# Performance work log

Measured on AMD Instinct MI355X. Metric: run time of the kernel, lower is better.

## Reference

```python
import math
import jax, jax.numpy as jnp
import numpy as np

N, T, D, H = 256, 128, 1024, 1024


def setup_inputs() -> dict:
    key = jax.random.key(0)
    k1, k2, k3, k4, k5 = jax.random.split(key, 5)
    x = jax.random.normal(k1, (N, T, D), dtype=jnp.float32)
    A = jax.random.normal(k2, (N, H, 4, 4), dtype=jnp.float32)
    Wx = jax.random.normal(k3, (D, 4 * H), dtype=jnp.float32) / math.sqrt(D)
    Wh = jax.random.normal(k4, (H, 4 * H), dtype=jnp.float32) / math.sqrt(H)
    Wattn = jax.random.normal(k5, (H, 4 * H), dtype=jnp.float32) / math.sqrt(H)
    b = jnp.zeros((4 * H,), dtype=jnp.float32)
    return {"x": x, "A": A, "Wx": Wx, "Wh": Wh, "Wattn": Wattn, "b": b}


def reference(x, A, Wx, Wh, Wattn, b):
    n, t, d = x.shape
    h = A.shape[1]
    A_flat = A.reshape(n, h, -1)            # (N, H, 16)
    h0 = A_flat.mean(axis=-1)               # mean over 4x4 grid
    c0 = h0
    scale = 1.0 / math.sqrt(h)

    def step(carry, xt):
        prev_h, prev_c = carry
        # scaled dot-product attention over the 16 spatial locations
        scores = jnp.einsum('nh,nhl->nl', prev_h, A_flat) * scale  # (N, 16)
        w = jax.nn.softmax(scores, axis=1)
        attn = jnp.einsum('nhl,nl->nh', A_flat, w)                 # (N, H)
        pre = xt @ Wx + prev_h @ Wh + attn @ Wattn + b             # (N, 4H)
        ai, af, ao, ag = jnp.split(pre, 4, axis=1)
        i = jax.nn.sigmoid(ai)
        f = jax.nn.sigmoid(af)
        o = jax.nn.sigmoid(ao)
        g = jnp.tanh(ag)
        next_c = f * prev_c + i * g
        next_h = o * jnp.tanh(next_c)
        return (next_h, next_c), next_h

    xs = jnp.swapaxes(x, 0, 1)               # (T, N, D)
    _, hs = jax.lax.scan(step, (h0, c0), xs)  # hs: (T, N, H)
    return jnp.swapaxes(hs, 0, 1)             # (N, T, H)
```

## Files before the change

### kernel.cpp

```cpp
#include <hip/hip_runtime.h>
#include <hip/hip_bf16.h>
#include <stdint.h>

#define N_ 256
#define T_ 128
#define D_ 1024
#define H_ 1024
#define FH_ 4096
#define K2_ 2048

typedef __bf16 bf16x8 __attribute__((ext_vector_type(8)));
typedef float f32x4 __attribute__((ext_vector_type(4)));

__global__ __launch_bounds__(256) void transpose_cast(
    const float* __restrict__ src, int cols,
    __hip_bfloat16* __restrict__ dst, int dst_stride, int dst_coloff)
{
    __shared__ float tile[32][33];
    int cb = blockIdx.x * 32, rb = blockIdx.y * 32;
    int tx = threadIdx.x, ty = threadIdx.y;
#pragma unroll
    for (int i = 0; i < 4; i++)
        tile[ty + i * 8][tx] = src[(size_t)(rb + ty + i * 8) * cols + cb + tx];
    __syncthreads();
#pragma unroll
    for (int i = 0; i < 4; i++)
        dst[(size_t)(cb + ty + i * 8) * dst_stride + dst_coloff + rb + tx] =
            __float2bfloat16(tile[tx][ty + i * 8]);
}

#define BM 64
#define BN 128
#define BK 64
#define BKP 72

__global__ __launch_bounds__(256) void gemm_x(
    const float* __restrict__ Xf,
    const __hip_bfloat16* __restrict__ BT,
    __hip_bfloat16* __restrict__ Cp, int t0)
{
    __shared__ __hip_bfloat16 Al[BM][BKP];
    __shared__ __hip_bfloat16 Bl[BN][BKP];
    const int tid = threadIdx.x;
    const int lane = tid & 63, wid = tid >> 6;
    const int m0 = blockIdx.y * BM, n0 = blockIdx.x * BN;
    const int wm = (wid >> 1) * 32, wn = (wid & 1) * 64;
    const int rs = tid >> 3, kc = (tid & 7) * 8;
    f32x4 acc[2][4] = {};

    for (int k0 = 0; k0 < D_; k0 += BK) {
#pragma unroll
        for (int p = 0; p < BM; p += 32) {
            int r = rs + p;
            int g = m0 + r;
            int nn = g & 255, tl = g >> 8;
            const float* s = Xf + ((size_t)nn * T_ + (t0 + tl)) * D_ + k0 + kc;
            float4 v0 = *reinterpret_cast<const float4*>(s);
            float4 v1 = *reinterpret_cast<const float4*>(s + 4);
            __hip_bfloat16 h8[8];
            h8[0] = __float2bfloat16(v0.x); h8[1] = __float2bfloat16(v0.y);
            h8[2] = __float2bfloat16(v0.z); h8[3] = __float2bfloat16(v0.w);
            h8[4] = __float2bfloat16(v1.x); h8[5] = __float2bfloat16(v1.y);
            h8[6] = __float2bfloat16(v1.z); h8[7] = __float2bfloat16(v1.w);
            *reinterpret_cast<int4*>(&Al[r][kc]) = *reinterpret_cast<const int4*>(h8);
        }
#pragma unroll
        for (int p = 0; p < BN; p += 32) {
            int r = rs + p;
            const __hip_bfloat16* s = BT + (size_t)(n0 + r) * D_ + k0 + kc;
            *reinterpret_cast<int4*>(&Bl[r][kc]) = *reinterpret_cast<const int4*>(s);
        }
        __syncthreads();
        const int ko = (lane >> 4) * 8;
#pragma unroll
        for (int kk = 0; kk < BK; kk += 32) {
            bf16x8 a0 = *reinterpret_cast<const bf16x8*>(&Al[wm + (lane & 15)][kk + ko]);
            bf16x8 a1 = *reinterpret_cast<const bf16x8*>(&Al[wm + 16 + (lane & 15)][kk + ko]);
#pragma unroll
            for (int ni = 0; ni < 4; ni++) {
                bf16x8 bq = *reinterpret_cast<const bf16x8*>(&Bl[wn + ni * 16 + (lane & 15)][kk + ko]);
                acc[0][ni] = __builtin_amdgcn_mfma_f32_16x16x32_bf16(a0, bq, acc[0][ni], 0, 0, 0);
                acc[1][ni] = __builtin_amdgcn_mfma_f32_16x16x32_bf16(a1, bq, acc[1][ni], 0, 0, 0);
            }
        }
        __syncthreads();
    }
    const int cr = (lane >> 4) * 4, ccol = lane & 15;
#pragma unroll
    for (int mi = 0; mi < 2; mi++)
#pragma unroll
        for (int ni = 0; ni < 4; ni++)
#pragma unroll
            for (int r = 0; r < 4; r++) {
                size_t idx = (size_t)(m0 + wm + mi * 16 + cr + r) * FH_ + (n0 + wn + ni * 16 + ccol);
                Cp[idx] = __float2bfloat16(acc[mi][ni][r]);
            }
}

__global__ __launch_bounds__(256) void abf_cast(
    const float* __restrict__ A, __hip_bfloat16* __restrict__ Abf)
{
    size_t i = ((size_t)blockIdx.x * 256 + threadIdx.x) * 4;
    float4 v = *reinterpret_cast<const float4*>(A + i);
    __hip_bfloat16 o[4];
    o[0] = __float2bfloat16(v.x); o[1] = __float2bfloat16(v.y);
    o[2] = __float2bfloat16(v.z); o[3] = __float2bfloat16(v.w);
    *reinterpret_cast<uint2*>(Abf + i) = *reinterpret_cast<uint2*>(o);
}

__global__ __launch_bounds__(256) void init_p(
    const float* __restrict__ A, float* __restrict__ cbuf,
    __hip_bfloat16* __restrict__ hb0)
{
    const int n = blockIdx.x, tid = threadIdx.x;
    float hv[4];
#pragma unroll
    for (int q = 0; q < 4; q++) {
        const float4* Ap = reinterpret_cast<const float4*>(A + ((size_t)n * H_ + tid * 4 + q) * 16);
        float4 q0 = Ap[0], q1 = Ap[1], q2 = Ap[2], q3 = Ap[3];
        float s = q0.x + q0.y + q0.z + q0.w + q1.x + q1.y + q1.z + q1.w
                + q2.x + q2.y + q2.z + q2.w + q3.x + q3.y + q3.z + q3.w;
        hv[q] = s * 0.0625f;
    }
    *reinterpret_cast<float4*>(cbuf + (size_t)n * H_ + tid * 4) = *reinterpret_cast<float4*>(hv);
    __hip_bfloat16 h4[4];
#pragma unroll
    for (int q = 0; q < 4; q++) h4[q] = __float2bfloat16(hv[q]);
    *reinterpret_cast<uint2*>(hb0 + (size_t)n * K2_ + tid * 4) = *reinterpret_cast<uint2*>(h4);
}

__global__ __launch_bounds__(256) void wattn2(
    __hip_bfloat16* __restrict__ hbt,
    const __hip_bfloat16* __restrict__ Abf)
{
    __shared__ float red[4][16];
    const int n = blockIdx.x, tid = threadIdx.x;
    const int lane = tid & 63, wv4 = tid >> 6;

    float h4[4];
    {
        uint2 hraw = *reinterpret_cast<const uint2*>(hbt + (size_t)n * K2_ + tid * 4);
        __hip_bfloat16 hb4[4];
        *reinterpret_cast<uint2*>(hb4) = hraw;
#pragma unroll
        for (int q = 0; q < 4; q++) h4[q] = __bfloat162float(hb4[q]);
    }
    bf16x8 a[4][2];
    const __hip_bfloat16* ap = Abf + ((size_t)n * H_ + tid * 4) * 16;
#pragma unroll
    for (int q = 0; q < 4; q++) {
        a[q][0] = *reinterpret_cast<const bf16x8*>(ap + q * 16);
        a[q][1] = *reinterpret_cast<const bf16x8*>(ap + q * 16 + 8);
    }
    float spv[16];
#pragma unroll
    for (int l = 0; l < 8; l++) {
        spv[l]     = h4[0] * (float)a[0][0][l] + h4[1] * (float)a[1][0][l]
                   + h4[2] * (float)a[2][0][l] + h4[3] * (float)a[3][0][l];
        spv[l + 8] = h4[0] * (float)a[0][1][l] + h4[1] * (float)a[1][1][l]
                   + h4[2] * (float)a[2][1][l] + h4[3] * (float)a[3][1][l];
    }
#pragma unroll
    for (int l = 0; l < 16; l++) {
        spv[l] += __shfl_xor(spv[l], 1);  spv[l] += __shfl_xor(spv[l], 2);
        spv[l] += __shfl_xor(spv[l], 4);  spv[l] += __shfl_xor(spv[l], 8);
        spv[l] += __shfl_xor(spv[l], 16); spv[l] += __shfl_xor(spv[l], 32);
    }
    if (lane == 0) {
#pragma unroll
        for (int l = 0; l < 16; l++) red[wv4][l] = spv[l];
    }
    __syncthreads();
    float w[16], se = 0.f;
    {
        float sc[16], m;
#pragma unroll
        for (int l = 0; l < 16; l++)
            sc[l] = (red[0][l] + red[1][l] + red[2][l] + red[3][l]) * 0.03125f;
        m = sc[0];
#pragma unroll
        for (int l = 1; l < 16; l++) m = fmaxf(m, sc[l]);
#pragma unroll
        for (int l = 0; l < 16; l++) { w[l] = __expf(sc[l] - m); se += w[l]; }
        float inv = 1.f / se;
#pragma unroll
        for (int l = 0; l < 16; l++) w[l] *= inv;
    }
    __hip_bfloat16 o4[4];
#pragma unroll
    for (int q = 0; q < 4; q++) {
        float s = 0.f;
#pragma unroll
        for (int l = 0; l < 8; l++) s += w[l] * (float)a[q][0][l];
#pragma unroll
        for (int l = 0; l < 8; l++) s += w[l + 8] * (float)a[q][1][l];
        o4[q] = __float2bfloat16(s);
    }
    *reinterpret_cast<uint2*>(hbt + (size_t)n * K2_ + H_ + tid * 4) =
        *reinterpret_cast<uint2*>(o4);
}

#define LDAp 136

__global__ __launch_bounds__(512) void step_gemm(
    const __hip_bfloat16* __restrict__ hb_in,
    __hip_bfloat16* __restrict__ hb_out,
    const __hip_bfloat16* __restrict__ W2T,
    const __hip_bfloat16* __restrict__ xp,
    const float* __restrict__ bias,
    float* __restrict__ cbuf,
    float* __restrict__ out, int t)
{
    __shared__ __align__(16) char smem[69632];
    float* pls = (float*)smem;

    const int tid = threadIdx.x;
    const int lane = tid & 63, wv = tid >> 6;
    const int bid = blockIdx.x;
    const int q = bid >> 3;
    const int ct = (bid & 7) + 8 * (q >> 2);
    const int r  = q & 3;
    const int hc0 = ct * 16, n0 = r * 64;
    const int rs = tid >> 4;
    const int kc = (tid & 15) * 8;
    const int l15 = lane & 15, ko8 = (lane >> 4) * 8;
    const int wm = (wv >> 1) * 16, wn = (wv & 1) * 32;

    const int gB0 = ((rs) >> 4) * 1024 + hc0 + (rs & 15);
    const int gB1 = ((rs + 32) >> 4) * 1024 + hc0 + ((rs + 32) & 15);
    const __hip_bfloat16* aS0 = hb_in + (size_t)(n0 + rs) * K2_ + kc;
    const __hip_bfloat16* aS1 = hb_in + (size_t)(n0 + rs + 32) * K2_ + kc;
    const __hip_bfloat16* bS0 = W2T + (size_t)gB0 * K2_ + kc;
    const __hip_bfloat16* bS1 = W2T + (size_t)gB1 * K2_ + kc;

    int4 ra0, ra1, rb0, rb1;
    auto LOAD = [&](int k0) {
        ra0 = *reinterpret_cast<const int4*>(aS0 + k0);
        ra1 = *reinterpret_cast<const int4*>(aS1 + k0);
        rb0 = *reinterpret_cast<const int4*>(bS0 + k0);
        rb1 = *reinterpret_cast<const int4*>(bS1 + k0);
    };
    auto WRITE = [&](int b) {
        __hip_bfloat16* Al = (__hip_bfloat16*)(smem + b * 17408);
        __hip_bfloat16* Bl = (__hip_bfloat16*)(smem + 34816 + b * 17408);
        *reinterpret_cast<int4*>(Al + rs * LDAp + kc) = ra0;
        *reinterpret_cast<int4*>(Al + (rs + 32) * LDAp + kc) = ra1;
        *reinterpret_cast<int4*>(Bl + rs * LDAp + kc) = rb0;
        *reinterpret_cast<int4*>(Bl + (rs + 32) * LDAp + kc) = rb1;
    };

    LOAD(0);
    WRITE(0);
    __syncthreads();

    f32x4 acc0{}, acc1{};
#pragma unroll 1
    for (int it = 0; it < 16; ++it) {
        if (it < 15) LOAD((it + 1) * 128);
        const int cur = it & 1;
        const __hip_bfloat16* pA  = (const __hip_bfloat16*)(smem + cur * 17408) + (wm + l15) * LDAp + ko8;
        const __hip_bfloat16* pB0 = (const __hip_bfloat16*)(smem + 34816 + cur * 17408) + (wn + l15) * LDAp + ko8;
        const __hip_bfloat16* pB1 = pB0 + 16 * LDAp;
#pragma unroll
        for (int kf = 0; kf < 4; kf++) {
            bf16x8 af = *reinterpret_cast<const bf16x8*>(pA + kf * 32);
            bf16x8 b0 = *reinterpret_cast<const bf16x8*>(pB0 + kf * 32);
            bf16x8 b1 = *reinterpret_cast<const bf16x8*>(pB1 + kf * 32);
            acc0 = __builtin_amdgcn_mfma_f32_16x16x32_bf16(af, b0, acc0, 0, 0, 0);
            acc1 = __builtin_amdgcn_mfma_f32_16x16x32_bf16(af, b1, acc1, 0, 0, 0);
        }
        __syncthreads();
        if (it < 15) {
            WRITE(cur ^ 1);
            __syncthreads();
        }
    }

    {
        const int cr = (lane >> 4) * 4;
#pragma unroll
        for (int r4 = 0; r4 < 4; r4++) {
            pls[(wm + cr + r4) * 68 + wn + l15]      = acc0[r4];
            pls[(wm + cr + r4) * 68 + wn + 16 + l15] = acc1[r4];
        }
    }
    __syncthreads();

    {
        const int n_l = tid >> 3, c2 = (tid & 7) * 2;
        const int nn = n0 + n_l;
        float hv2[2], cv2[2];
        const size_t cbase = (size_t)nn * H_ + hc0 + c2;
        float2 cold = *reinterpret_cast<const float2*>(cbuf + cbase);
        cv2[0] = cold.x; cv2[1] = cold.y;
#pragma unroll
        for (int cc = 0; cc < 2; cc++) {
            const int c = c2 + cc;
            float pre[4];
#pragma unroll
            for (int s = 0; s < 4; s++) {
                const int gj = s * 1024 + hc0 + c;
                pre[s] = pls[n_l * 68 + s * 16 + c]
                       + __bfloat162float(xp[(size_t)nn * FH_ + gj]) + bias[gj];
            }
            float iv = 1.f / (1.f + __expf(-pre[0]));
            float fv = 1.f / (1.f + __expf(-pre[1]));
            float ov = 1.f / (1.f + __expf(-pre[2]));
            float gx = fminf(fmaxf(pre[3], -20.f), 20.f);
            float eg = __expf(2.f * gx);
            float gv = (eg - 1.f) / (eg + 1.f);
            float c2v = fv * cv2[cc] + iv * gv;
            cv2[cc] = c2v;
            float cx = fminf(fmaxf(c2v, -20.f), 20.f);
            float ec = __expf(2.f * cx);
            hv2[cc] = ov * (ec - 1.f) / (ec + 1.f);
        }
        *reinterpret_cast<float2*>(cbuf + cbase) = make_float2(cv2[0], cv2[1]);
        *reinterpret_cast<float2*>(out + ((size_t)nn * T_ + t) * H_ + hc0 + c2) =
            make_float2(hv2[0], hv2[1]);
        __hip_bfloat16 h2[2];
        h2[0] = __float2bfloat16(hv2[0]);
        h2[1] = __float2bfloat16(hv2[1]);
        *reinterpret_cast<uint32_t*>(hb_out + (size_t)nn * K2_ + hc0 + c2) =
            *reinterpret_cast<uint32_t*>(h2);
    }
}

extern "C" void kernel_launch(void* const* d_in, const int* in_sizes, int n_in,
                              void* d_out, int out_size, void* d_ws, size_t ws_size,
                              hipStream_t stream)
{
    const float* x     = (const float*)d_in[0];
    const float* A     = (const float*)d_in[1];
    const float* Wx    = (const float*)d_in[2];
    const float* Wh    = (const float*)d_in[3];
    const float* Wattn = (const float*)d_in[4];
    const float* b     = (const float*)d_in[5];
    float* out = (float*)d_out;
    char* ws = (char*)d_ws;
    dim3 tb(32, 8);

    const size_t SZ_W2T = (size_t)FH_ * K2_ * 2;
    const size_t SZ_WxT = (size_t)FH_ * D_ * 2;
    const size_t SZ_Abf = (size_t)N_ * H_ * 16 * 2;
    const size_t SZ_HB  = (size_t)N_ * K2_ * 2;
    const size_t SZ_C   = (size_t)N_ * H_ * 4;
    const size_t SZ_XPT = (size_t)N_ * FH_ * 2;

    size_t off = 0;
    __hip_bfloat16* W2T = (__hip_bfloat16*)(ws + off); off += SZ_W2T;
    __hip_bfloat16* WxT = (__hip_bfloat16*)(ws + off); off += SZ_WxT;
    __hip_bfloat16* Abf = (__hip_bfloat16*)(ws + off); off += SZ_Abf;
    __hip_bfloat16* hbA = (__hip_bfloat16*)(ws + off); off += SZ_HB;
    __hip_bfloat16* hbB = (__hip_bfloat16*)(ws + off); off += SZ_HB;
    float* cbuf = (float*)(ws + off); off += SZ_C;
    __hip_bfloat16* xpb = (__hip_bfloat16*)(ws + off);

    size_t rem = (ws_size > off) ? (ws_size - off) : 0;
    int TC = 64;
    while (TC > 1 && (size_t)TC * SZ_XPT > rem) TC >>= 1;

    transpose_cast<<<dim3(FH_ / 32, H_ / 32), tb, 0, stream>>>(Wh, FH_, W2T, K2_, 0);
    transpose_cast<<<dim3(FH_ / 32, H_ / 32), tb, 0, stream>>>(Wattn, FH_, W2T, K2_, H_);
    transpose_cast<<<dim3(FH_ / 32, D_ / 32), tb, 0, stream>>>(Wx, FH_, WxT, D_, 0);
    abf_cast<<<dim3((N_ * H_ * 16) / 1024), 256, 0, stream>>>(A, Abf);
    init_p<<<N_, 256, 0, stream>>>(A, cbuf, hbA);

    __hip_bfloat16* hbp[2] = {hbA, hbB};
    for (int t0 = 0; t0 < T_; t0 += TC) {
        int tc = (T_ - t0 < TC) ? (T_ - t0) : TC;
        gemm_x<<<dim3(FH_ / BN, tc * N_ / BM), 256, 0, stream>>>(x, WxT, xpb, t0);
        for (int tl = 0; tl < tc; tl++) {
            int t = t0 + tl;
            wattn2<<<N_, 256, 0, stream>>>(hbp[t & 1], Abf);
            step_gemm<<<dim3(256), 512, 0, stream>>>(
                hbp[t & 1], hbp[(t + 1) & 1], W2T,
                xpb + (size_t)tl * N_ * FH_, b, cbuf, out, t);
        }
    }
}
```

Baseline: 3.113 ms.

## Precompute A·Wattn per batch and fuse attention into step kernel

Uses linearity to precompute AW = A_flat^T·Wattn per batch (N×4H×16) once, so each step's attention contribution becomes a 16-term weighted sum of AW with the softmax weights. This halves the recurrent GEMM K dimension from 2048 to 1024. It also removes the separate per-step wattn kernel: the step kernel emits partial attention scores for the next step, and the next step reduces them. The trade-off is a large extra per-step read of AW (256×4096×16 bf16) in the epilogue. The WaT scratch also aliases the xp buffer, which is safe only because aw_gemm runs before gemm_x.

```diff
diff --git a/kernel.cpp b/kernel.cpp
--- a/kernel.cpp
+++ b/kernel.cpp
@@ -7,7 +7,6 @@
 #define D_ 1024
 #define H_ 1024
 #define FH_ 4096
-#define K2_ 2048
 
 typedef __bf16 bf16x8 __attribute__((ext_vector_type(8)));
 typedef float f32x4 __attribute__((ext_vector_type(4)));
@@ -97,6 +96,55 @@
             }
 }
 
+__global__ __launch_bounds__(256) void aw_gemm(
+    const float* __restrict__ A, const __hip_bfloat16* __restrict__ WaT,
+    __hip_bfloat16* __restrict__ AW)
+{
+    __shared__ __hip_bfloat16 Al[16][72];
+    __shared__ __hip_bfloat16 Bl[128][72];
+    const int tid = threadIdx.x, lane = tid & 63, wv = tid >> 6;
+    const int n = blockIdx.y, j0 = blockIdx.x * 128;
+    const int rs = tid >> 3, kc = (tid & 7) * 8;
+    f32x4 acc[2] = {};
+    for (int k0 = 0; k0 < 1024; k0 += 64) {
+        {
+            int h = tid >> 2, lq = (tid & 3) * 4;
+            float4 v = *reinterpret_cast<const float4*>(A + ((size_t)n * 1024 + k0 + h) * 16 + lq);
+            Al[lq + 0][h] = __float2bfloat16(v.x);
+            Al[lq + 1][h] = __float2bfloat16(v.y);
+            Al[lq + 2][h] = __float2bfloat16(v.z);
+            Al[lq + 3][h] = __float2bfloat16(v.w);
+        }
+#pragma unroll
+        for (int p = 0; p < 128; p += 32) {
+            int r = rs + p;
+            *reinterpret_cast<int4*>(&Bl[r][kc]) =
+                *reinterpret_cast<const int4*>(WaT + (size_t)(j0 + r) * 1024 + k0 + kc);
+        }
+        __syncthreads();
+        const int ko = (lane >> 4) * 8;
+#pragma unroll
+        for (int kk = 0; kk < 64; kk += 32) {
+            bf16x8 a0 = *reinterpret_cast<const bf16x8*>(&Al[lane & 15][kk + ko]);
+#pragma unroll
+            for (int nf = 0; nf < 2; nf++) {
+                bf16x8 bq = *reinterpret_cast<const bf16x8*>(&Bl[wv * 32 + nf * 16 + (lane & 15)][kk + ko]);
+                acc[nf] = __builtin_amdgcn_mfma_f32_16x16x32_bf16(a0, bq, acc[nf], 0, 0, 0);
+            }
+        }
+        __syncthreads();
+    }
+    const int cr = (lane >> 4) * 4, cc = lane & 15;
+#pragma unroll
+    for (int nf = 0; nf < 2; nf++) {
+        __hip_bfloat16 t4[4];
+#pragma unroll
+        for (int r = 0; r < 4; r++) t4[r] = __float2bfloat16(acc[nf][r]);
+        *reinterpret_cast<uint2*>(AW + ((size_t)n * 4096 + j0 + wv * 32 + nf * 16 + cc) * 16 + cr) =
+            *reinterpret_cast<uint2*>(t4);
+    }
+}
+
 __global__ __launch_bounds__(256) void abf_cast(
     const float* __restrict__ A, __hip_bfloat16* __restrict__ Abf)
 {
@@ -108,58 +156,37 @@
     *reinterpret_cast<uint2*>(Abf + i) = *reinterpret_cast<uint2*>(o);
 }
 
-__global__ __launch_bounds__(256) void init_p(
+__global__ __launch_bounds__(256) void init_s(
     const float* __restrict__ A, float* __restrict__ cbuf,
-    __hip_bfloat16* __restrict__ hb0)
-{
+    __hip_bfloat16* __restrict__ hb0, float* __restrict__ sp0)
+{
+    __shared__ float red[4][16];
     const int n = blockIdx.x, tid = threadIdx.x;
+    const int lane = tid & 63, wvv = tid >> 6;
+    float a[4][16];
     float hv[4];
 #pragma unroll
     for (int q = 0; q < 4; q++) {
         const float4* Ap = reinterpret_cast<const float4*>(A + ((size_t)n * H_ + tid * 4 + q) * 16);
         float4 q0 = Ap[0], q1 = Ap[1], q2 = Ap[2], q3 = Ap[3];
-        float s = q0.x + q0.y + q0.z + q0.w + q1.x + q1.y + q1.z + q1.w
-                + q2.x + q2.y + q2.z + q2.w + q3.x + q3.y + q3.z + q3.w;
+        a[q][0] = q0.x; a[q][1] = q0.y; a[q][2] = q0.z; a[q][3] = q0.w;
+        a[q][4] = q1.x; a[q][5] = q1.y; a[q][6] = q1.z; a[q][7] = q1.w;
+        a[q][8] = q2.x; a[q][9] = q2.y; a[q][10] = q2.z; a[q][11] = q2.w;
+        a[q][12] = q3.x; a[q][13] = q3.y; a[q][14] = q3.z; a[q][15] = q3.w;
+        float s = 0.f;
+#pragma unroll
+        for (int l = 0; l < 16; l++) s += a[q][l];
         hv[q] = s * 0.0625f;
     }
     *reinterpret_cast<float4*>(cbuf + (size_t)n * H_ + tid * 4) = *reinterpret_cast<float4*>(hv);
     __hip_bfloat16 h4[4];
 #pragma unroll
     for (int q = 0; q < 4; q++) h4[q] = __float2bfloat16(hv[q]);
-    *reinterpret_cast<uint2*>(hb0 + (size_t)n * K2_ + tid * 4) = *reinterpret_cast<uint2*>(h4);
-}
-
-__global__ __launch_bounds__(256) void wattn2(
-    __hip_bfloat16* __restrict__ hbt,
-    const __hip_bfloat16* __restrict__ Abf)
-{
-    __shared__ float red[4][16];
-    const int n = blockIdx.x, tid = threadIdx.x;
-    const int lane = tid & 63, wv4 = tid >> 6;
-
-    float h4[4];
-    {
-        uint2 hraw = *reinterpret_cast<const uint2*>(hbt + (size_t)n * K2_ + tid * 4);
-        __hip_bfloat16 hb4[4];
-        *reinterpret_cast<uint2*>(hb4) = hraw;
-#pragma unroll
-        for (int q = 0; q < 4; q++) h4[q] = __bfloat162float(hb4[q]);
-    }
-    bf16x8 a[4][2];
-    const __hip_bfloat16* ap = Abf + ((size_t)n * H_ + tid * 4) * 16;
-#pragma unroll
-    for (int q = 0; q < 4; q++) {
-        a[q][0] = *reinterpret_cast<const bf16x8*>(ap + q * 16);
-        a[q][1] = *reinterpret_cast<const bf16x8*>(ap + q * 16 + 8);
-    }
+    *reinterpret_cast<uint2*>(hb0 + (size_t)n * H_ + tid * 4) = *reinterpret_cast<uint2*>(h4);
     float spv[16];
 #pragma unroll
-    for (int l = 0; l < 8; l++) {
-        spv[l]     = h4[0] * (float)a[0][0][l] + h4[1] * (float)a[1][0][l]
-                   + h4[2] * (float)a[2][0][l] + h4[3] * (float)a[3][0][l];
-        spv[l + 8] = h4[0] * (float)a[0][1][l] + h4[1] * (float)a[1][1][l]
-                   + h4[2] * (float)a[2][1][l] + h4[3] * (float)a[3][1][l];
-    }
+    for (int l = 0; l < 16; l++)
+        spv[l] = hv[0] * a[0][l] + hv[1] * a[1][l] + hv[2] * a[2][l] + hv[3] * a[3][l];
 #pragma unroll
     for (int l = 0; l < 16; l++) {
         spv[l] += __shfl_xor(spv[l], 1);  spv[l] += __shfl_xor(spv[l], 2);
@@ -168,50 +195,36 @@
     }
     if (lane == 0) {
 #pragma unroll
-        for (int l = 0; l < 16; l++) red[wv4][l] = spv[l];
+        for (int l = 0; l < 16; l++) red[wvv][l] = spv[l];
     }
     __syncthreads();
-    float w[16], se = 0.f;
-    {
-        float sc[16], m;
-#pragma unroll
-        for (int l = 0; l < 16; l++)
-            sc[l] = (red[0][l] + red[1][l] + red[2][l] + red[3][l]) * 0.03125f;
-        m = sc[0];
-#pragma unroll
-        for (int l = 1; l < 16; l++) m = fmaxf(m, sc[l]);
-#pragma unroll
-        for (int l = 0; l < 16; l++) { w[l] = __expf(sc[l] - m); se += w[l]; }
-        float inv = 1.f / se;
-#pragma unroll
-        for (int l = 0; l < 16; l++) w[l] *= inv;
-    }
-    __hip_bfloat16 o4[4];
-#pragma unroll
-    for (int q = 0; q < 4; q++) {
-        float s = 0.f;
-#pragma unroll
-        for (int l = 0; l < 8; l++) s += w[l] * (float)a[q][0][l];
-#pragma unroll
-        for (int l = 0; l < 8; l++) s += w[l + 8] * (float)a[q][1][l];
-        o4[q] = __float2bfloat16(s);
-    }
-    *reinterpret_cast<uint2*>(hbt + (size_t)n * K2_ + H_ + tid * 4) =
-        *reinterpret_cast<uint2*>(o4);
+    float* spn = sp0 + (size_t)n * 1024;
+    if (tid < 16)
+        spn[tid] = red[0][tid] + red[1][tid] + red[2][tid] + red[3][tid];
+#pragma unroll
+    for (int j = 0; j < 4; j++) {
+        int idx = 16 + tid * 4 + j;
+        if (idx < 1024) spn[idx] = 0.f;
+    }
 }
 
 #define LDAp 136
 
-__global__ __launch_bounds__(512) void step_gemm(
+__global__ __launch_bounds__(512) void step_fused(
     const __hip_bfloat16* __restrict__ hb_in,
     __hip_bfloat16* __restrict__ hb_out,
-    const __hip_bfloat16* __restrict__ W2T,
+    const __hip_bfloat16* __restrict__ WhT,
+    const __hip_bfloat16* __restrict__ AW,
+    const __hip_bfloat16* __restrict__ Abf,
     const __hip_bfloat16* __restrict__ xp,
     const float* __restrict__ bias,
     float* __restrict__ cbuf,
+    const float* __restrict__ sp_in,
+    float* __restrict__ sp_out,
     float* __restrict__ out, int t)
 {
     __shared__ __align__(16) char smem[69632];
+    __shared__ float wl[64][16];
     float* pls = (float*)smem;
 
     const int tid = threadIdx.x;
@@ -226,12 +239,12 @@
     const int l15 = lane & 15, ko8 = (lane >> 4) * 8;
     const int wm = (wv >> 1) * 16, wn = (wv & 1) * 32;
 
-    const int gB0 = ((rs) >> 4) * 1024 + hc0 + (rs & 15);
-    const int gB1 = ((rs + 32) >> 4) * 1024 + hc0 + ((rs + 32) & 15);
-    const __hip_bfloat16* aS0 = hb_in + (size_t)(n0 + rs) * K2_ + kc;
-    const __hip_bfloat16* aS1 = hb_in + (size_t)(n0 + rs + 32) * K2_ + kc;
-    const __hip_bfloat16* bS0 = W2T + (size_t)gB0 * K2_ + kc;
-    const __hip_bfloat16* bS1 = W2T + (size_t)gB1 * K2_ + kc;
+    const int j0 = (rs >> 4) * 1024 + hc0 + (rs & 15);
+    const int j1 = ((rs + 32) >> 4) * 1024 + hc0 + ((rs + 32) & 15);
+    const __hip_bfloat16* aS0 = hb_in + (size_t)(n0 + rs) * H_ + kc;
+    const __hip_bfloat16* aS1 = hb_in + (size_t)(n0 + rs + 32) * H_ + kc;
+    const __hip_bfloat16* bS0 = WhT + (size_t)j0 * H_ + kc;
+    const __hip_bfloat16* bS1 = WhT + (size_t)j1 * H_ + kc;
 
     int4 ra0, ra1, rb0, rb1;
     auto LOAD = [&](int k0) {
@@ -249,14 +262,36 @@
         *reinterpret_cast<int4*>(Bl + (rs + 32) * LDAp + kc) = rb1;
     };
 
+    {
+        const int row8 = tid >> 3, l2 = (tid & 7) * 2;
+        const float* spn = sp_in + (size_t)(n0 + row8) * 1024 + l2;
+        float s0 = 0.f, s1 = 0.f;
+#pragma unroll 8
+        for (int cj = 0; cj < 64; cj++) {
+            float2 v = *reinterpret_cast<const float2*>(spn + cj * 16);
+            s0 += v.x; s1 += v.y;
+        }
+        s0 *= 0.03125f; s1 *= 0.03125f;
+        float m = fmaxf(s0, s1);
+        m = fmaxf(m, __shfl_xor(m, 1));
+        m = fmaxf(m, __shfl_xor(m, 2));
+        m = fmaxf(m, __shfl_xor(m, 4));
+        float e0 = __expf(s0 - m), e1 = __expf(s1 - m);
+        float se = e0 + e1;
+        se += __shfl_xor(se, 1); se += __shfl_xor(se, 2); se += __shfl_xor(se, 4);
+        float inv = 1.f / se;
+        wl[row8][l2] = e0 * inv;
+        wl[row8][l2 + 1] = e1 * inv;
+    }
+
     LOAD(0);
     WRITE(0);
     __syncthreads();
 
     f32x4 acc0{}, acc1{};
 #pragma unroll 1
-    for (int it = 0; it < 16; ++it) {
-        if (it < 15) LOAD((it + 1) * 128);
+    for (int it = 0; it < 8; ++it) {
+        if (it < 7) LOAD((it + 1) * 128);
         const int cur = it & 1;
         const __hip_bfloat16* pA  = (const __hip_bfloat16*)(smem + cur * 17408) + (wm + l15) * LDAp + ko8;
         const __hip_bfloat16* pB0 = (const __hip_bfloat16*)(smem + 34816 + cur * 17408) + (wn + l15) * LDAp + ko8;
@@ -270,7 +305,7 @@
             acc1 = __builtin_amdgcn_mfma_f32_16x16x32_bf16(af, b1, acc1, 0, 0, 0);
         }
         __syncthreads();
-        if (it < 15) {
+        if (it < 7) {
             WRITE(cur ^ 1);
             __syncthreads();
         }
@@ -289,24 +324,41 @@
     {
         const int n_l = tid >> 3, c2 = (tid & 7) * 2;
         const int nn = n0 + n_l;
+        float w[16];
+#pragma unroll
+        for (int l = 0; l < 16; l++) w[l] = wl[n_l][l];
+
+        float pre[4][2];
+#pragma unroll
+        for (int s = 0; s < 4; s++) {
+            const int gj = s * 1024 + hc0 + c2;
+            __hip_bfloat16 xb[2];
+            *reinterpret_cast<uint32_t*>(xb) =
+                *reinterpret_cast<const uint32_t*>(xp + (size_t)nn * FH_ + gj);
+            const __hip_bfloat16* awp = AW + ((size_t)nn * FH_ + gj) * 16;
+#pragma unroll
+            for (int cc = 0; cc < 2; cc++) {
+                bf16x8 w0 = *reinterpret_cast<const bf16x8*>(awp + cc * 16);
+                bf16x8 w1 = *reinterpret_cast<const bf16x8*>(awp + cc * 16 + 8);
+                float aw = 0.f;
+#pragma unroll
+                for (int l = 0; l < 8; l++) aw += w[l] * (float)w0[l];
+#pragma unroll
+                for (int l = 0; l < 8; l++) aw += w[l + 8] * (float)w1[l];
+                pre[s][cc] = pls[n_l * 68 + s * 16 + c2 + cc]
+                           + __bfloat162float(xb[cc]) + bias[gj + cc] + aw;
+            }
+        }
         float hv2[2], cv2[2];
         const size_t cbase = (size_t)nn * H_ + hc0 + c2;
         float2 cold = *reinterpret_cast<const float2*>(cbuf + cbase);
         cv2[0] = cold.x; cv2[1] = cold.y;
 #pragma unroll
         for (int cc = 0; cc < 2; cc++) {
-            const int c = c2 + cc;
-            float pre[4];
-#pragma unroll
-            for (int s = 0; s < 4; s++) {
-                const int gj = s * 1024 + hc0 + c;
-                pre[s] = pls[n_l * 68 + s * 16 + c]
-                       + __bfloat162float(xp[(size_t)nn * FH_ + gj]) + bias[gj];
-            }
-            float iv = 1.f / (1.f + __expf(-pre[0]));
-            float fv = 1.f / (1.f + __expf(-pre[1]));
-            float ov = 1.f / (1.f + __expf(-pre[2]));
-            float gx = fminf(fmaxf(pre[3], -20.f), 20.f);
+            float iv = 1.f / (1.f + __expf(-pre[0][cc]));
+            float fv = 1.f / (1.f + __expf(-pre[1][cc]));
+            float ov = 1.f / (1.f + __expf(-pre[2][cc]));
+            float gx = fminf(fmaxf(pre[3][cc], -20.f), 20.f);
             float eg = __expf(2.f * gx);
             float gv = (eg - 1.f) / (eg + 1.f);
             float c2v = fv * cv2[cc] + iv * gv;
@@ -321,8 +373,33 @@
         __hip_bfloat16 h2[2];
         h2[0] = __float2bfloat16(hv2[0]);
         h2[1] = __float2bfloat16(hv2[1]);
-        *reinterpret_cast<uint32_t*>(hb_out + (size_t)nn * K2_ + hc0 + c2) =
+        *reinterpret_cast<uint32_t*>(hb_out + (size_t)nn * H_ + hc0 + c2) =
             *reinterpret_cast<uint32_t*>(h2);
+
+        const __hip_bfloat16* ap = Abf + ((size_t)nn * H_ + hc0 + c2) * 16;
+        bf16x8 a00 = *reinterpret_cast<const bf16x8*>(ap);
+        bf16x8 a01 = *reinterpret_cast<const bf16x8*>(ap + 8);
+        bf16x8 a10 = *reinterpret_cast<const bf16x8*>(ap + 16);
+        bf16x8 a11 = *reinterpret_cast<const bf16x8*>(ap + 24);
+        float spv[16];
+#pragma unroll
+        for (int l = 0; l < 8; l++) {
+            spv[l]     = hv2[0] * (float)a00[l] + hv2[1] * (float)a10[l];
+            spv[l + 8] = hv2[0] * (float)a01[l] + hv2[1] * (float)a11[l];
+        }
+#pragma unroll
+        for (int l = 0; l < 16; l++) {
+            spv[l] += __shfl_xor(spv[l], 1);
+            spv[l] += __shfl_xor(spv[l], 2);
+            spv[l] += __shfl_xor(spv[l], 4);
+        }
+        if ((tid & 7) == 0) {
+            float* d = sp_out + ((size_t)nn * 64 + ct) * 16;
+            *reinterpret_cast<float4*>(d)      = *reinterpret_cast<float4*>(&spv[0]);
+            *reinterpret_cast<float4*>(d + 4)  = *reinterpret_cast<float4*>(&spv[4]);
+            *reinterpret_cast<float4*>(d + 8)  = *reinterpret_cast<float4*>(&spv[8]);
+            *reinterpret_cast<float4*>(d + 12) = *reinterpret_cast<float4*>(&spv[12]);
+        }
     }
 }
 
@@ -340,42 +417,50 @@
     char* ws = (char*)d_ws;
     dim3 tb(32, 8);
 
-    const size_t SZ_W2T = (size_t)FH_ * K2_ * 2;
+    const size_t SZ_WhT = (size_t)FH_ * H_ * 2;
     const size_t SZ_WxT = (size_t)FH_ * D_ * 2;
+    const size_t SZ_AW  = (size_t)N_ * FH_ * 16 * 2;
     const size_t SZ_Abf = (size_t)N_ * H_ * 16 * 2;
-    const size_t SZ_HB  = (size_t)N_ * K2_ * 2;
+    const size_t SZ_HB  = (size_t)N_ * H_ * 2;
     const size_t SZ_C   = (size_t)N_ * H_ * 4;
+    const size_t SZ_SP  = (size_t)N_ * 64 * 16 * 4;
     const size_t SZ_XPT = (size_t)N_ * FH_ * 2;
 
     size_t off = 0;
-    __hip_bfloat16* W2T = (__hip_bfloat16*)(ws + off); off += SZ_W2T;
+    __hip_bfloat16* WhT = (__hip_bfloat16*)(ws + off); off += SZ_WhT;
     __hip_bfloat16* WxT = (__hip_bfloat16*)(ws + off); off += SZ_WxT;
+    __hip_bfloat16* AW  = (__hip_bfloat16*)(ws + off); off += SZ_AW;
     __hip_bfloat16* Abf = (__hip_bfloat16*)(ws + off); off += SZ_Abf;
     __hip_bfloat16* hbA = (__hip_bfloat16*)(ws + off); off += SZ_HB;
     __hip_bfloat16* hbB = (__hip_bfloat16*)(ws + off); off += SZ_HB;
     float* cbuf = (float*)(ws + off); off += SZ_C;
+    float* sp0  = (float*)(ws + off); off += SZ_SP;
+    float* sp1  = (float*)(ws + off); off += SZ_SP;
     __hip_bfloat16* xpb = (__hip_bfloat16*)(ws + off);
+    __hip_bfloat16* WaT = xpb;
 
     size_t rem = (ws_size > off) ? (ws_size - off) : 0;
     int TC = 64;
     while (TC > 1 && (size_t)TC * SZ_XPT > rem) TC >>= 1;
 
-    transpose_cast<<<dim3(FH_ / 32, H_ / 32), tb, 0, stream>>>(Wh, FH_, W2T, K2_, 0);
-    transpose_cast<<<dim3(FH_ / 32, H_ / 32), tb, 0, stream>>>(Wattn, FH_, W2T, K2_, H_);
+    transpose_cast<<<dim3(FH_ / 32, H_ / 32), tb, 0, stream>>>(Wh, FH_, WhT, H_, 0);
+    transpose_cast<<<dim3(FH_ / 32, H_ / 32), tb, 0, stream>>>(Wattn, FH_, WaT, H_, 0);
+    aw_gemm<<<dim3(32, N_), 256, 0, stream>>>(A, WaT, AW);
     transpose_cast<<<dim3(FH_ / 32, D_ / 32), tb, 0, stream>>>(Wx, FH_, WxT, D_, 0);
     abf_cast<<<dim3((N_ * H_ * 16) / 1024), 256, 0, stream>>>(A, Abf);
-    init_p<<<N_, 256, 0, stream>>>(A, cbuf, hbA);
+    init_s<<<N_, 256, 0, stream>>>(A, cbuf, hbA, sp0);
 
     __hip_bfloat16* hbp[2] = {hbA, hbB};
+    float* spp[2] = {sp0, sp1};
     for (int t0 = 0; t0 < T_; t0 += TC) {
         int tc = (T_ - t0 < TC) ? (T_ - t0) : TC;
         gemm_x<<<dim3(FH_ / BN, tc * N_ / BM), 256, 0, stream>>>(x, WxT, xpb, t0);
         for (int tl = 0; tl < tc; tl++) {
             int t = t0 + tl;
-            wattn2<<<N_, 256, 0, stream>>>(hbp[t & 1], Abf);
-            step_gemm<<<dim3(256), 512, 0, stream>>>(
-                hbp[t & 1], hbp[(t + 1) & 1], W2T,
-                xpb + (size_t)tl * N_ * FH_, b, cbuf, out, t);
-        }
-    }
-}
+            step_fused<<<dim3(256), 512, 0, stream>>>(
+                hbp[t & 1], hbp[(t + 1) & 1], WhT, AW, Abf,
+                xpb + (size_t)tl * N_ * FH_, b, cbuf,
+                spp[t & 1], spp[(t + 1) & 1], out, t);
+        }
+    }
+}
```

Result: no change. 3.170 ms (+1.8%).

## Fuse input projection GEMM into step kernel as extra lookahead blocks

Applied to the files above, without the earlier changes.

Replaces the chunked upfront x@Wx GEMM with a ring buffer of 8 timesteps. The step kernel gets 128 extra blocks that compute the input projection for step t+4 while the recurrent GEMM for step t runs. Only the first 4 steps are precomputed by a separate launch. This is meant to hide the input-projection GEMM inside the underutilized per-step launches, at the cost of sharing CUs between the two workloads. The extra blocks use a simple unpipelined tile loop that casts fp32 to bf16 on the fly.

```diff
diff --git a/kernel.cpp b/kernel.cpp
--- a/kernel.cpp
+++ b/kernel.cpp
@@ -8,6 +8,7 @@
 #define H_ 1024
 #define FH_ 4096
 #define K2_ 2048
+#define LOOKAHEAD 4
 
 typedef __bf16 bf16x8 __attribute__((ext_vector_type(8)));
 typedef float f32x4 __attribute__((ext_vector_type(4)));
@@ -206,17 +207,84 @@
     const __hip_bfloat16* __restrict__ hb_in,
     __hip_bfloat16* __restrict__ hb_out,
     const __hip_bfloat16* __restrict__ W2T,
-    const __hip_bfloat16* __restrict__ xp,
+    const __hip_bfloat16* __restrict__ xpb,
     const float* __restrict__ bias,
     float* __restrict__ cbuf,
-    float* __restrict__ out, int t)
+    float* __restrict__ out,
+    const float* __restrict__ Xf,
+    const __hip_bfloat16* __restrict__ WxT,
+    int t)
 {
     __shared__ __align__(16) char smem[69632];
-    float* pls = (float*)smem;
 
     const int tid = threadIdx.x;
     const int lane = tid & 63, wv = tid >> 6;
     const int bid = blockIdx.x;
+
+    if (bid >= 256) {
+        const int tf = t + LOOKAHEAD;
+        if (tf >= T_) return;
+        __hip_bfloat16* xW = (__hip_bfloat16*)xpb + (size_t)(tf & 7) * N_ * FH_;
+        __hip_bfloat16* Al = (__hip_bfloat16*)smem;
+        __hip_bfloat16* Bl = (__hip_bfloat16*)(smem + 9216);
+        const int e = bid - 256;
+        const int n0x = (e & 31) * 128;
+        const int m0x = (e >> 5) * 64;
+        const int wm = (wv >> 2) * 32, wn = (wv & 3) * 32;
+        const int l15 = lane & 15, ko = (lane >> 4) * 8;
+        const int rs2 = tid >> 3, kc2 = (tid & 7) * 8;
+        const int rs3 = tid >> 2, kc3 = (tid & 3) * 16;
+        f32x4 acc[2][2] = {};
+
+        for (int k0 = 0; k0 < D_; k0 += 64) {
+            {
+                const float* s = Xf + ((size_t)(m0x + rs2) * T_ + tf) * D_ + k0 + kc2;
+                float4 v0 = *reinterpret_cast<const float4*>(s);
+                float4 v1 = *reinterpret_cast<const float4*>(s + 4);
+                __hip_bfloat16 h8[8];
+                h8[0] = __float2bfloat16(v0.x); h8[1] = __float2bfloat16(v0.y);
+                h8[2] = __float2bfloat16(v0.z); h8[3] = __float2bfloat16(v0.w);
+                h8[4] = __float2bfloat16(v1.x); h8[5] = __float2bfloat16(v1.y);
+                h8[6] = __float2bfloat16(v1.z); h8[7] = __float2bfloat16(v1.w);
+                *reinterpret_cast<int4*>(Al + rs2 * 72 + kc2) =
+                    *reinterpret_cast<const int4*>(h8);
+            }
+            {
+                const __hip_bfloat16* s = WxT + (size_t)(n0x + rs3) * D_ + k0 + kc3;
+                *reinterpret_cast<int4*>(Bl + rs3 * 72 + kc3) =
+                    *reinterpret_cast<const int4*>(s);
+                *reinterpret_cast<int4*>(Bl + rs3 * 72 + kc3 + 8) =
+                    *reinterpret_cast<const int4*>(s + 8);
+            }
+            __syncthreads();
+#pragma unroll
+            for (int kk = 0; kk < 64; kk += 32) {
+                bf16x8 a0 = *reinterpret_cast<const bf16x8*>(Al + (wm + l15) * 72 + kk + ko);
+                bf16x8 a1 = *reinterpret_cast<const bf16x8*>(Al + (wm + 16 + l15) * 72 + kk + ko);
+                bf16x8 b0 = *reinterpret_cast<const bf16x8*>(Bl + (wn + l15) * 72 + kk + ko);
+                bf16x8 b1 = *reinterpret_cast<const bf16x8*>(Bl + (wn + 16 + l15) * 72 + kk + ko);
+                acc[0][0] = __builtin_amdgcn_mfma_f32_16x16x32_bf16(a0, b0, acc[0][0], 0, 0, 0);
+                acc[0][1] = __builtin_amdgcn_mfma_f32_16x16x32_bf16(a0, b1, acc[0][1], 0, 0, 0);
+                acc[1][0] = __builtin_amdgcn_mfma_f32_16x16x32_bf16(a1, b0, acc[1][0], 0, 0, 0);
+                acc[1][1] = __builtin_amdgcn_mfma_f32_16x16x32_bf16(a1, b1, acc[1][1], 0, 0, 0);
+            }
+            __syncthreads();
+        }
+        const int cr = (lane >> 4) * 4;
+#pragma unroll
+        for (int mi = 0; mi < 2; mi++)
+#pragma unroll
+            for (int ni = 0; ni < 2; ni++)
+#pragma unroll
+                for (int r4 = 0; r4 < 4; r4++)
+                    xW[(size_t)(m0x + wm + mi * 16 + cr + r4) * FH_ +
+                       (n0x + wn + ni * 16 + l15)] = __float2bfloat16(acc[mi][ni][r4]);
+        return;
+    }
+
+    float* pls = (float*)smem;
+    const __hip_bfloat16* xp = xpb + (size_t)(t & 7) * N_ * FH_;
+
     const int q = bid >> 3;
     const int ct = (bid & 7) + 8 * (q >> 2);
     const int r  = q & 3;
@@ -345,7 +413,7 @@
     const size_t SZ_Abf = (size_t)N_ * H_ * 16 * 2;
     const size_t SZ_HB  = (size_t)N_ * K2_ * 2;
     const size_t SZ_C   = (size_t)N_ * H_ * 4;
-    const size_t SZ_XPT = (size_t)N_ * FH_ * 2;
+    const size_t SZ_XPR = (size_t)8 * N_ * FH_ * 2;
 
     size_t off = 0;
     __hip_bfloat16* W2T = (__hip_bfloat16*)(ws + off); off += SZ_W2T;
@@ -354,28 +422,19 @@
     __hip_bfloat16* hbA = (__hip_bfloat16*)(ws + off); off += SZ_HB;
     __hip_bfloat16* hbB = (__hip_bfloat16*)(ws + off); off += SZ_HB;
     float* cbuf = (float*)(ws + off); off += SZ_C;
-    __hip_bfloat16* xpb = (__hip_bfloat16*)(ws + off);
-
-    size_t rem = (ws_size > off) ? (ws_size - off) : 0;
-    int TC = 64;
-    while (TC > 1 && (size_t)TC * SZ_XPT > rem) TC >>= 1;
+    __hip_bfloat16* xpb = (__hip_bfloat16*)(ws + off); off += SZ_XPR;
 
     transpose_cast<<<dim3(FH_ / 32, H_ / 32), tb, 0, stream>>>(Wh, FH_, W2T, K2_, 0);
     transpose_cast<<<dim3(FH_ / 32, H_ / 32), tb, 0, stream>>>(Wattn, FH_, W2T, K2_, H_);
     transpose_cast<<<dim3(FH_ / 32, D_ / 32), tb, 0, stream>>>(Wx, FH_, WxT, D_, 0);
     abf_cast<<<dim3((N_ * H_ * 16) / 1024), 256, 0, stream>>>(A, Abf);
     init_p<<<N_, 256, 0, stream>>>(A, cbuf, hbA);
+    gemm_x<<<dim3(FH_ / BN, LOOKAHEAD * N_ / BM), 256, 0, stream>>>(x, WxT, xpb, 0);
 
     __hip_bfloat16* hbp[2] = {hbA, hbB};
-    for (int t0 = 0; t0 < T_; t0 += TC) {
-        int tc = (T_ - t0 < TC) ? (T_ - t0) : TC;
-        gemm_x<<<dim3(FH_ / BN, tc * N_ / BM), 256, 0, stream>>>(x, WxT, xpb, t0);
-        for (int tl = 0; tl < tc; tl++) {
-            int t = t0 + tl;
-            wattn2<<<N_, 256, 0, stream>>>(hbp[t & 1], Abf);
-            step_gemm<<<dim3(256), 512, 0, stream>>>(
-                hbp[t & 1], hbp[(t + 1) & 1], W2T,
-                xpb + (size_t)tl * N_ * FH_, b, cbuf, out, t);
-        }
-    }
-}
+    for (int t = 0; t < T_; t++) {
+        wattn2<<<N_, 256, 0, stream>>>(hbp[t & 1], Abf);
+        step_gemm<<<dim3(384), 512, 0, stream>>>(
+            hbp[t & 1], hbp[(t + 1) & 1], W2T, xpb, b, cbuf, out, x, WxT, t);
+    }
+}
```

Measured after the change: 4.020 ms. 1.29x slower.

## Retile recurrent step GEMM into smaller blocks and swizzle gemm_x block order

Applied to the files above, without the earlier changes.

The per-timestep recurrent GEMM is retiled from 256 blocks of 512 threads (64x64 output tiles) to 512 blocks of 256 threads (32 batch rows x 64 gate columns). Each wave now loads one gate's 16-column B fragment and reuses it across two 16-row A fragments. The goal is to spread the small, latency-bound step across more CUs and shrink shared memory per block, at the cost of each weight tile being fetched by twice as many row blocks. Separately, gemm_x remaps linear block indices so that groups of neighbouring blocks share A rows and B columns, aiming for better L2 reuse.

```diff
diff --git a/kernel.cpp b/kernel.cpp
--- a/kernel.cpp
+++ b/kernel.cpp
@@ -43,7 +43,10 @@
     __shared__ __hip_bfloat16 Bl[BN][BKP];
     const int tid = threadIdx.x;
     const int lane = tid & 63, wid = tid >> 6;
-    const int m0 = blockIdx.y * BM, n0 = blockIdx.x * BN;
+    const int lin = blockIdx.y * gridDim.x + blockIdx.x;
+    const int cti = (lin & 7) + 8 * ((lin >> 3) & 3);
+    const int mti = lin >> 5;
+    const int m0 = mti * BM, n0 = cti * BN;
     const int wm = (wid >> 1) * 32, wn = (wid & 1) * 64;
     const int rs = tid >> 3, kc = (tid & 7) * 8;
     f32x4 acc[2][4] = {};
@@ -202,7 +205,7 @@
 
 #define LDAp 136
 
-__global__ __launch_bounds__(512) void step_gemm(
+__global__ __launch_bounds__(256) void step_gemm(
     const __hip_bfloat16* __restrict__ hb_in,
     __hip_bfloat16* __restrict__ hb_out,
     const __hip_bfloat16* __restrict__ W2T,
@@ -211,42 +214,45 @@
     float* __restrict__ cbuf,
     float* __restrict__ out, int t)
 {
-    __shared__ __align__(16) char smem[69632];
+    __shared__ __align__(16) char smem[52224];
     float* pls = (float*)smem;
 
     const int tid = threadIdx.x;
     const int lane = tid & 63, wv = tid >> 6;
     const int bid = blockIdx.x;
-    const int q = bid >> 3;
-    const int ct = (bid & 7) + 8 * (q >> 2);
-    const int r  = q & 3;
-    const int hc0 = ct * 16, n0 = r * 64;
+    const int k = bid >> 3;
+    const int ct = (bid & 7) + 8 * (k & 7);
+    const int r  = k >> 3;
+    const int hc0 = ct * 16, n0 = r * 32;
     const int rs = tid >> 4;
     const int kc = (tid & 15) * 8;
     const int l15 = lane & 15, ko8 = (lane >> 4) * 8;
-    const int wm = (wv >> 1) * 16, wn = (wv & 1) * 32;
-
-    const int gB0 = ((rs) >> 4) * 1024 + hc0 + (rs & 15);
-    const int gB1 = ((rs + 32) >> 4) * 1024 + hc0 + ((rs + 32) & 15);
+
     const __hip_bfloat16* aS0 = hb_in + (size_t)(n0 + rs) * K2_ + kc;
-    const __hip_bfloat16* aS1 = hb_in + (size_t)(n0 + rs + 32) * K2_ + kc;
-    const __hip_bfloat16* bS0 = W2T + (size_t)gB0 * K2_ + kc;
-    const __hip_bfloat16* bS1 = W2T + (size_t)gB1 * K2_ + kc;
-
-    int4 ra0, ra1, rb0, rb1;
+    const __hip_bfloat16* aS1 = hb_in + (size_t)(n0 + rs + 16) * K2_ + kc;
+    const __hip_bfloat16* bS0 = W2T + (size_t)(0 * 1024 + hc0 + rs) * K2_ + kc;
+    const __hip_bfloat16* bS1 = W2T + (size_t)(1 * 1024 + hc0 + rs) * K2_ + kc;
+    const __hip_bfloat16* bS2 = W2T + (size_t)(2 * 1024 + hc0 + rs) * K2_ + kc;
+    const __hip_bfloat16* bS3 = W2T + (size_t)(3 * 1024 + hc0 + rs) * K2_ + kc;
+
+    int4 ra0, ra1, rb0, rb1, rb2, rb3;
     auto LOAD = [&](int k0) {
         ra0 = *reinterpret_cast<const int4*>(aS0 + k0);
         ra1 = *reinterpret_cast<const int4*>(aS1 + k0);
         rb0 = *reinterpret_cast<const int4*>(bS0 + k0);
         rb1 = *reinterpret_cast<const int4*>(bS1 + k0);
+        rb2 = *reinterpret_cast<const int4*>(bS2 + k0);
+        rb3 = *reinterpret_cast<const int4*>(bS3 + k0);
     };
     auto WRITE = [&](int b) {
-        __hip_bfloat16* Al = (__hip_bfloat16*)(smem + b * 17408);
-        __hip_bfloat16* Bl = (__hip_bfloat16*)(smem + 34816 + b * 17408);
+        __hip_bfloat16* Al = (__hip_bfloat16*)(smem + b * 8704);
+        __hip_bfloat16* Bl = (__hip_bfloat16*)(smem + 17408 + b * 17408);
         *reinterpret_cast<int4*>(Al + rs * LDAp + kc) = ra0;
-        *reinterpret_cast<int4*>(Al + (rs + 32) * LDAp + kc) = ra1;
+        *reinterpret_cast<int4*>(Al + (rs + 16) * LDAp + kc) = ra1;
         *reinterpret_cast<int4*>(Bl + rs * LDAp + kc) = rb0;
-        *reinterpret_cast<int4*>(Bl + (rs + 32) * LDAp + kc) = rb1;
+        *reinterpret_cast<int4*>(Bl + (rs + 16) * LDAp + kc) = rb1;
+        *reinterpret_cast<int4*>(Bl + (rs + 32) * LDAp + kc) = rb2;
+        *reinterpret_cast<int4*>(Bl + (rs + 48) * LDAp + kc) = rb3;
     };
 
     LOAD(0);
@@ -258,16 +264,16 @@
     for (int it = 0; it < 16; ++it) {
         if (it < 15) LOAD((it + 1) * 128);
         const int cur = it & 1;
-        const __hip_bfloat16* pA  = (const __hip_bfloat16*)(smem + cur * 17408) + (wm + l15) * LDAp + ko8;
-        const __hip_bfloat16* pB0 = (const __hip_bfloat16*)(smem + 34816 + cur * 17408) + (wn + l15) * LDAp + ko8;
-        const __hip_bfloat16* pB1 = pB0 + 16 * LDAp;
+        const __hip_bfloat16* pA = (const __hip_bfloat16*)(smem + cur * 8704) + l15 * LDAp + ko8;
+        const __hip_bfloat16* pB = (const __hip_bfloat16*)(smem + 17408 + cur * 17408)
+                                   + (wv * 16 + l15) * LDAp + ko8;
 #pragma unroll
         for (int kf = 0; kf < 4; kf++) {
-            bf16x8 af = *reinterpret_cast<const bf16x8*>(pA + kf * 32);
-            bf16x8 b0 = *reinterpret_cast<const bf16x8*>(pB0 + kf * 32);
-            bf16x8 b1 = *reinterpret_cast<const bf16x8*>(pB1 + kf * 32);
-            acc0 = __builtin_amdgcn_mfma_f32_16x16x32_bf16(af, b0, acc0, 0, 0, 0);
-            acc1 = __builtin_amdgcn_mfma_f32_16x16x32_bf16(af, b1, acc1, 0, 0, 0);
+            bf16x8 a0 = *reinterpret_cast<const bf16x8*>(pA + kf * 32);
+            bf16x8 a1 = *reinterpret_cast<const bf16x8*>(pA + 16 * LDAp + kf * 32);
+            bf16x8 bq = *reinterpret_cast<const bf16x8*>(pB + kf * 32);
+            acc0 = __builtin_amdgcn_mfma_f32_16x16x32_bf16(a0, bq, acc0, 0, 0, 0);
+            acc1 = __builtin_amdgcn_mfma_f32_16x16x32_bf16(a1, bq, acc1, 0, 0, 0);
         }
         __syncthreads();
         if (it < 15) {
@@ -280,8 +286,8 @@
         const int cr = (lane >> 4) * 4;
 #pragma unroll
         for (int r4 = 0; r4 < 4; r4++) {
-            pls[(wm + cr + r4) * 68 + wn + l15]      = acc0[r4];
-            pls[(wm + cr + r4) * 68 + wn + 16 + l15] = acc1[r4];
+            pls[(cr + r4) * 68 + wv * 16 + l15]      = acc0[r4];
+            pls[(16 + cr + r4) * 68 + wv * 16 + l15] = acc1[r4];
         }
     }
     __syncthreads();
@@ -373,7 +379,7 @@
         for (int tl = 0; tl < tc; tl++) {
             int t = t0 + tl;
             wattn2<<<N_, 256, 0, stream>>>(hbp[t & 1], Abf);
-            step_gemm<<<dim3(256), 512, 0, stream>>>(
+            step_gemm<<<dim3(512), 256, 0, stream>>>(
                 hbp[t & 1], hbp[(t + 1) & 1], W2T,
                 xpb + (size_t)tl * N_ * FH_, b, cbuf, out, t);
         }
```

Measured after the change: 3.085 ms (median of 2 runs). Within noise of the previous version (-0.9%).
